# Kernel optimization log

Hardware: AMD Instinct MI355X
Metric: run time of the kernel (lower is better)

## Reference

```python
import jax, jax.numpy as jnp
import numpy as np

MAX_DIST = 20
N_HEADS = 8
LN_EPS = 1e-5


def _layer_norm(x, g, b):
    mu = jnp.mean(x, axis=-1, keepdims=True)
    var = jnp.var(x, axis=-1, keepdims=True)
    return (x - mu) / jnp.sqrt(var + LN_EPS) * g + b


def setup_inputs() -> dict:
    key = jax.random.key(0)
    ks = jax.random.split(key, 12)
    B, N, D, H, F = 8, 1024, 768, N_HEADS, 1024
    w = lambda k, *sh: (jax.random.normal(k, sh, jnp.float32) * 0.02)
    return {
        "x": jax.random.normal(ks[0], (B, N, D), jnp.float32),
        "node_mask": jnp.ones((B, N), jnp.int32),
        "centers": jnp.arange(B * N, dtype=jnp.float32).reshape(B, N),
        "types": jax.random.randint(ks[1], (B, N), 0, 2, jnp.int32),
        # params (torch Linear weights stored transposed as [in, out])
        "qkv_w": w(ks[2], D, 3 * D), "qkv_b": jnp.zeros((3 * D,), jnp.float32),
        "out_w": w(ks[3], D, D), "out_b": jnp.zeros((D,), jnp.float32),
        "ff1_w": w(ks[4], D, F), "ff1_b": jnp.zeros((F,), jnp.float32),
        "ff2_w": w(ks[5], F, D), "ff2_b": jnp.zeros((D,), jnp.float32),
        "ln1_g": jnp.ones((D,), jnp.float32), "ln1_b": jnp.zeros((D,), jnp.float32),
        "ln2_g": jnp.ones((D,), jnp.float32), "ln2_b": jnp.zeros((D,), jnp.float32),
        "rel_emb": w(ks[6], 2 * MAX_DIST + 1, H),  # relative-distance bias table
        "tt": w(ks[7], H, 2, 2),                   # type-pair bias table
    }


def reference(x, node_mask, centers, types,
              qkv_w, qkv_b, out_w, out_b,
              ff1_w, ff1_b, ff2_w, ff2_b,
              ln1_g, ln1_b, ln2_g, ln2_b,
              rel_emb, tt):
    B, N, D = x.shape
    H = rel_emb.shape[1]
    Dh = D // H

    qkv = x @ qkv_w + qkv_b                       # [B,N,3D]
    q, k, v = jnp.split(qkv, 3, axis=-1)
    split = lambda t: t.reshape(B, N, H, Dh).transpose(0, 2, 1, 3)  # [B,H,N,Dh]
    q, k, v = split(q), split(k), split(v)

    scores = jnp.einsum("bhid,bhjd->bhij", q, k) / np.sqrt(Dh).astype(np.float32)

    # relative-position bias: bucket clamped distance into [0, 2*max_dist]
    dist = centers[:, :, None] - centers[:, None, :]              # [B,N,N]
    idx = jnp.round(jnp.clip(dist, -MAX_DIST, MAX_DIST) + MAX_DIST).astype(jnp.int32)
    rb = rel_emb[idx].transpose(0, 3, 1, 2)                       # [B,H,N,N]

    # type-pair bias
    ti = jnp.broadcast_to(types[:, :, None], (B, N, N))
    tj = jnp.broadcast_to(types[:, None, :], (B, N, N))
    tb = tt[:, ti, tj].transpose(1, 0, 2, 3)                      # [B,H,N,N]

    scores = scores + rb + tb
    mask = node_mask[:, None, None, :]                            # [B,1,1,N]
    scores = jnp.where(mask == 0, -jnp.inf, scores)
    att = jax.nn.softmax(scores, axis=-1)
    att = jnp.nan_to_num(att, nan=0.0)

    y = jnp.einsum("bhij,bhjd->bhid", att, v)
    y = y.transpose(0, 2, 1, 3).reshape(B, N, D)
    y = y @ out_w + out_b

    x = _layer_norm(x + y, ln1_g, ln1_b)
    ff = jax.nn.gelu(x @ ff1_w + ff1_b, approximate=False) @ ff2_w + ff2_b
    x = _layer_norm(x + ff, ln2_g, ln2_b)
    return x
```

## Files before the change

### kernel.cpp

```cpp
#include <hip/hip_runtime.h>

typedef short short8 __attribute__((ext_vector_type(8)));
typedef unsigned short ushort8v __attribute__((ext_vector_type(8)));
typedef float f32x4 __attribute__((ext_vector_type(4)));

static __device__ __forceinline__ unsigned short f2b(float f) {
    unsigned int u = __builtin_bit_cast(unsigned int, f);
    unsigned int r = (u + 0x7fffu + ((u >> 16) & 1u)) >> 16;
    return (unsigned short)r;
}
static __device__ __forceinline__ float b2f(unsigned short u) {
    return __builtin_bit_cast(float, (unsigned int)u << 16);
}
static __device__ __forceinline__ float exp2v(float x) {
    float r;
    asm("v_exp_f32 %0, %1" : "=v"(r) : "v"(x));
    return r;
}
static __device__ __forceinline__ unsigned cvt_pk_bf16(float lo, float hi) {
    unsigned r;
    asm("v_cvt_pk_bf16_f32 %0, %1, %2" : "=v"(r) : "v"(lo), "v"(hi));
    return r;
}

__device__ __forceinline__ void gload16(void* lds, const void* g) {
    __builtin_amdgcn_global_load_lds(
        (const __attribute__((address_space(1))) void*)g,
        (__attribute__((address_space(3))) void*)lds, 16, 0, 0);
}

#define L2E 1.4426950408889634f

__global__ __launch_bounds__(256) void prep_kernel(
    const float* __restrict__ x, unsigned short* __restrict__ xb,
    const float* __restrict__ qkv_w, unsigned short* __restrict__ qwT,
    const float* __restrict__ out_w, unsigned short* __restrict__ owT,
    const float* __restrict__ ff1_w, unsigned short* __restrict__ f1T,
    const float* __restrict__ ff2_w, unsigned short* __restrict__ f2T) {
    const int bx = blockIdx.x;
    const int tid = threadIdx.x;
    if (bx < 6144) {
        int i = bx * 256 + tid;
        float4 f = ((const float4*)x)[i];
        ushort4 u;
        u.x = f2b(f.x); u.y = f2b(f.y); u.z = f2b(f.z); u.w = f2b(f.w);
        ((ushort4*)xb)[i] = u;
        return;
    }
    __shared__ float t[32][33];
    int rb = bx - 6144;
    const float* W; unsigned short* Wt; int K, N;
    if (rb < 1728)      { W = qkv_w; Wt = qwT; K = 768;  N = 2304; }
    else if (rb < 2304) { rb -= 1728; W = out_w; Wt = owT; K = 768;  N = 768; }
    else if (rb < 3072) { rb -= 2304; W = ff1_w; Wt = f1T; K = 768;  N = 1024; }
    else                { rb -= 3072; W = ff2_w; Wt = f2T; K = 1024; N = 768; }
    const int nbl = N / 32;
    const int nb = (rb % nbl) * 32, kb = (rb / nbl) * 32;
    const int tx = tid & 31, ty = tid >> 5;
#pragma unroll
    for (int i = 0; i < 32; i += 8)
        t[ty + i][tx] = W[(size_t)(kb + ty + i) * N + nb + tx];
    __syncthreads();
#pragma unroll
    for (int i = 0; i < 32; i += 8)
        Wt[(size_t)(nb + ty + i) * K + kb + tx] = f2b(t[tx][ty + i]);
}

template <int EPI>
__global__ __launch_bounds__(512, 4) void gemm2p(
    const unsigned short* __restrict__ A, const unsigned short* __restrict__ Bt,
    const float* __restrict__ bias, float* __restrict__ outf,
    unsigned short* __restrict__ outb, unsigned short* __restrict__ q_o,
    unsigned short* __restrict__ k_o, unsigned short* __restrict__ v_o,
    int N, int K, int ntn, int NT) {
    __shared__ unsigned short a_lds[2][8192];
    __shared__ unsigned short b_lds[2][8192];
    const int tid = threadIdx.x;
    const int wave = tid >> 6, lane = tid & 63;
    const int lr = lane & 15, lg = lane >> 4;
    const int wm = wave >> 2, wn = wave & 3;
    const int nwg = gridDim.x;
    const int orig = blockIdx.x;
    const int swz = (orig & 7) * (nwg >> 3) + (orig >> 3);
    const int tm = swz / ntn, tn = swz % ntn;

    const unsigned short* srcA[2];
    const unsigned short* srcB[2];
#pragma unroll
    for (int i = 0; i < 2; ++i) {
        int g = i * 512 + tid;
        int row = g >> 3, sl = g & 7;
        int colg = sl ^ (row & 7);
        srcA[i] = A + (size_t)(tm * 128 + row) * K + colg * 8;
        srcB[i] = Bt + (size_t)(tn * 128 + row) * K + colg * 8;
    }
    auto stage = [&](int buf, int k0) {
#pragma unroll
        for (int i = 0; i < 2; ++i) {
            gload16(&a_lds[buf][i * 4096 + wave * 512], srcA[i] + k0);
            gload16(&b_lds[buf][i * 4096 + wave * 512], srcB[i] + k0);
        }
    };

    f32x4 acc[4][2] = {};

    stage(0, 0);
    asm volatile("s_waitcnt vmcnt(0)" ::: "memory");
    __builtin_amdgcn_s_barrier();

    for (int t = 0; t < NT; ++t) {
        const int buf = t & 1;
        if (t + 1 < NT) stage(buf ^ 1, (t + 1) * 64);
#pragma unroll
        for (int ks = 0; ks < 2; ++ks) {
            short8 af[4], bfr[2];
#pragma unroll
            for (int mf = 0; mf < 4; ++mf) {
                int row = wm * 64 + mf * 16 + lr;
                int slot = (ks * 4 + lg) ^ (row & 7);
                af[mf] = *(const short8*)&a_lds[buf][row * 64 + slot * 8];
            }
#pragma unroll
            for (int nf = 0; nf < 2; ++nf) {
                int row = wn * 32 + nf * 16 + lr;
                int slot = (ks * 4 + lg) ^ (row & 7);
                bfr[nf] = *(const short8*)&b_lds[buf][row * 64 + slot * 8];
            }
#pragma unroll
            for (int mf = 0; mf < 4; ++mf)
#pragma unroll
                for (int nf = 0; nf < 2; ++nf)
                    acc[mf][nf] = __builtin_amdgcn_mfma_f32_16x16x32_bf16(af[mf], bfr[nf], acc[mf][nf], 0, 0, 0);
        }
        asm volatile("s_waitcnt vmcnt(0)" ::: "memory");
        __builtin_amdgcn_s_barrier();
    }

#pragma unroll
    for (int nf = 0; nf < 2; ++nf) {
        int gc = tn * 128 + wn * 32 + nf * 16 + lr;
        float bv = bias[gc];
        int part = 0, h = 0, dh = 0;
        if constexpr (EPI == 3) {
            part = gc / 768;
            int cc = gc - part * 768;
            h = cc / 96;
            dh = cc - h * 96;
        }
#pragma unroll
        for (int mf = 0; mf < 4; ++mf) {
            int grb = tm * 128 + wm * 64 + mf * 16 + lg * 4;
            if constexpr (EPI == 3) {
                int b = grb >> 10, n2 = grb & 1023;
                size_t bh = (size_t)(b * 8 + h);
                if (part == 2) {
                    ushort4 wv;
                    wv.x = f2b(acc[mf][nf][0] + bv);
                    wv.y = f2b(acc[mf][nf][1] + bv);
                    wv.z = f2b(acc[mf][nf][2] + bv);
                    wv.w = f2b(acc[mf][nf][3] + bv);
                    *(ushort4*)&v_o[(bh * 96 + dh) * 1024 + n2] = wv;
                } else {
                    unsigned short* dst = (part == 0) ? q_o : k_o;
                    float sc = (part == 0) ? 0.14724445f : 1.f;
#pragma unroll
                    for (int r = 0; r < 4; ++r)
                        dst[(bh * 1024 + n2 + r) * 96 + dh] = f2b((acc[mf][nf][r] + bv) * sc);
                }
            } else {
#pragma unroll
                for (int r = 0; r < 4; ++r) {
                    int gr = grb + r;
                    float v = acc[mf][nf][r] + bv;
                    if constexpr (EPI == 0) {
                        outf[(size_t)gr * N + gc] = v;
                    } else if constexpr (EPI == 1) {
                        outb[(size_t)gr * N + gc] = f2b(v);
                    } else {
                        float gl = 0.5f * v * (1.f + erff(v * 0.70710678f));
                        outb[(size_t)gr * N + gc] = f2b(gl);
                    }
                }
            }
        }
    }
}

__global__ __launch_bounds__(512, 4) void attn_kernel(
    const unsigned short* __restrict__ Qb, const unsigned short* __restrict__ Kb,
    const unsigned short* __restrict__ Vt, const float* __restrict__ centers,
    const int* __restrict__ types, const int* __restrict__ nmask,
    const float* __restrict__ tt, const float* __restrict__ rel_emb,
    unsigned short* __restrict__ Y) {
    __shared__ unsigned short kv_lds[2 * 12288];
    __shared__ unsigned short p_lds[8 * 1024];
    __shared__ float c_lds[1024];
    __shared__ unsigned int bab_lds[1024];
    __shared__ float rel_lds[41];
    __shared__ float cjmm_lds[32];

    const int tid = threadIdx.x;
    const int wave = tid >> 6, lane = tid & 63;
    const int lr = lane & 15, lg = lane >> 4;
    const int bh = blockIdx.x, qb = blockIdx.y;
    const int b = bh >> 3, h = bh & 7;
    const int q0 = qb * 128 + wave * 16;
    const size_t kvbase = (size_t)bh * 1024 * 96;

    c_lds[tid] = centers[b * 1024 + tid];
    c_lds[tid + 512] = centers[b * 1024 + 512 + tid];
    if (tid < 41) rel_lds[tid] = rel_emb[tid * 8 + h] * L2E;
    {
        const float t00 = tt[h * 4], t01 = tt[h * 4 + 1];
        const float t10 = tt[h * 4 + 2], t11 = tt[h * 4 + 3];
#pragma unroll
        for (int i = 0; i < 2; ++i) {
            int j = tid + i * 512;
            int tj = types[b * 1024 + j];
            int mk = nmask[b * 1024 + j];
            float bA = L2E * (t00 + (t01 - t00) * tj) + (mk ? 0.f : -1e30f);
            float bB = L2E * ((t10 - t00) + (t11 - t01 - t10 + t00) * tj);
            bab_lds[j] = (unsigned)f2b(bA) | ((unsigned)f2b(bB) << 16);
        }
    }

    const unsigned short* sbase[3];
    int sstep[3];
#pragma unroll
    for (int it = 0; it < 3; ++it) {
        int g = it * 512 + tid;
        if (g < 768) {
            int ks = g >> 8, rem = g & 255, pr = rem >> 3, sl = rem & 7;
            int so = sl ^ (pr & 7);
            int r = ((so >> 2) << 5) + pr, oct = so & 3;
            sbase[it] = Kb + kvbase + (size_t)r * 96 + ks * 32 + oct * 8;
            sstep[it] = 64 * 96;
        } else {
            int gv = g - 768, pr = gv >> 3, sl = gv & 7;
            int so = sl ^ (pr & 7);
            sbase[it] = Vt + (size_t)(bh * 96 + pr) * 1024 + so * 8;
            sstep[it] = 64;
        }
    }
    auto stage = [&](int bufb, int kt) {
        unsigned short* dst = kv_lds + bufb * 12288;
#pragma unroll
        for (int it = 0; it < 3; ++it)
            gload16(dst + it * 4096 + wave * 512, sbase[it] + (size_t)kt * sstep[it]);
    };

    short8 qa[3];
#pragma unroll
    for (int ks = 0; ks < 3; ++ks)
        qa[ks] = *(const short8*)&Qb[kvbase + (size_t)(q0 + lr) * 96 + ks * 32 + lg * 8];
    short8 qa3 = {};
    {
        int ti0 = types[b * 1024 + q0 + lr];
        if (lg == 0) {
            qa3[0] = (short)0x3F80;
            qa3[1] = ti0 ? (short)0x3F80 : (short)0;
        }
    }
    const float ci20 = centers[b * 1024 + q0 + lr] + 20.f;
    float cimax20 = ci20, cimin20 = ci20;
#pragma unroll
    for (int off = 1; off < 16; off <<= 1) {
        cimax20 = fmaxf(cimax20, __shfl_xor(cimax20, off));
        cimin20 = fminf(cimin20, __shfl_xor(cimin20, off));
    }

    float m_s = -3e30f, l_s = 0.f;
    f32x4 oacc[6] = {};
    unsigned* p32 = (unsigned*)&p_lds[wave * 1024];

    stage(0, 0);
    asm volatile("s_waitcnt lgkmcnt(0)" ::: "memory");
    __builtin_amdgcn_s_barrier();

    if (tid < 256) {
        int ktt = tid >> 4;
        float4 cv = *(const float4*)&c_lds[ktt * 64 + (tid & 15) * 4];
        float mn = fminf(fminf(cv.x, cv.y), fminf(cv.z, cv.w));
        float mx = fmaxf(fmaxf(cv.x, cv.y), fmaxf(cv.z, cv.w));
#pragma unroll
        for (int off = 1; off < 16; off <<= 1) {
            mn = fminf(mn, __shfl_xor(mn, off));
            mx = fmaxf(mx, __shfl_xor(mx, off));
        }
        if ((tid & 15) == 0) { cjmm_lds[ktt] = mn; cjmm_lds[16 + ktt] = mx; }
    }
    asm volatile("s_waitcnt lgkmcnt(0)" ::: "memory");
    const float rel0v = rel_lds[0], rel40v = rel_lds[40];

    for (int kt = 0; kt < 16; ++kt) {
        const int buf = kt & 1;
        if (kt < 15) {
            stage(buf ^ 1, kt + 1);
            asm volatile("s_waitcnt vmcnt(3)" ::: "memory");
        } else {
            asm volatile("s_waitcnt vmcnt(0)" ::: "memory");
        }
        __builtin_amdgcn_s_barrier();
        const unsigned short* kv = kv_lds + buf * 12288;

        f32x4 s[4] = {};
#pragma unroll
        for (int jf = 0; jf < 4; ++jf) {
            int pr = ((jf & 1) << 4) + lr;
            int slp = (((jf >> 1) << 2) + lg) ^ (lr & 7);
#pragma unroll
            for (int ks = 0; ks < 3; ++ks) {
                short8 kf = *(const short8*)&kv[ks * 2048 + pr * 64 + slp * 8];
                s[jf] = __builtin_amdgcn_mfma_f32_16x16x32_bf16(kf, qa[ks], s[jf], 0, 0, 0);
            }
            unsigned vb = bab_lds[kt * 64 + jf * 16 + lr];
            short8 kf3 = {};
            if (lg == 0) {
                kf3[0] = (short)(vb & 0xffffu);
                kf3[1] = (short)(vb >> 16);
            }
            s[jf] = __builtin_amdgcn_mfma_f32_16x16x32_bf16(kf3, qa3, s[jf], 0, 0, 0);
        }

        float re_eff;
        {
            float cjmn = cjmm_lds[kt], cjmx = cjmm_lds[16 + kt];
            bool flatHi = (cimin20 - cjmx >= 40.f);
            bool flatLo = (cimax20 - cjmn <= 0.f);
            if (flatHi || flatLo) {
                re_eff = flatHi ? rel40v : rel0v;
            } else {
                re_eff = 0.f;
#pragma unroll
                for (int jf = 0; jf < 4; ++jf) {
                    float4 cj4 = *(const float4*)&c_lds[kt * 64 + jf * 16 + lg * 4];
                    float cjl[4] = {cj4.x, cj4.y, cj4.z, cj4.w};
#pragma unroll
                    for (int r = 0; r < 4; ++r) {
                        float idxf = __builtin_amdgcn_fmed3f(ci20 - cjl[r], 0.f, 40.f);
                        s[jf][r] += rel_lds[(int)rintf(idxf)];
                    }
                }
            }
        }

        {
            float mlr = s[0][0];
#pragma unroll
            for (int jf = 0; jf < 4; ++jf)
#pragma unroll
                for (int r = 0; r < 4; ++r) mlr = fmaxf(mlr, s[jf][r]);
            float mb = m_s - re_eff;
            if (!__all(mlr <= mb + 8.f)) {
                float mx = fmaxf(mlr, __shfl_xor(mlr, 16));
                mx = fmaxf(mx, __shfl_xor(mx, 32));
                mx += re_eff;
                float mn = fmaxf(m_s, mx);
                float al = exp2v(m_s - mn);
                m_s = mn;
                l_s *= al;
#pragma unroll
                for (int r = 0; r < 4; ++r) {
                    float alr = __shfl(al, lg * 4 + r);
#pragma unroll
                    for (int nf = 0; nf < 6; ++nf) oacc[nf][r] *= alr;
                }
                mb = m_s - re_eff;
            }
            float ls = 0.f;
#pragma unroll
            for (int jf = 0; jf < 4; ++jf)
#pragma unroll
                for (int r = 0; r < 4; ++r) {
                    s[jf][r] = exp2v(s[jf][r] - mb);
                    ls += s[jf][r];
                }
            ls += __shfl_xor(ls, 16);
            ls += __shfl_xor(ls, 32);
            l_s += ls;
        }

#pragma unroll
        for (int jf = 0; jf < 4; ++jf) {
            uint2 w2;
            w2.x = cvt_pk_bf16(s[jf][0], s[jf][1]);
            w2.y = cvt_pk_bf16(s[jf][2], s[jf][3]);
            int gsw = ((jf * 4 + lg) ^ (lr & 14)) * 2;
            *(uint2*)&p32[lr * 32 + gsw] = w2;
        }
        asm volatile("s_waitcnt lgkmcnt(0)" ::: "memory");
        short8 pa[2];
#pragma unroll
        for (int js = 0; js < 2; ++js) {
            int gsw = (((js * 8 + lg * 2) ^ (lr & 14))) * 2;
            pa[js] = *(const short8*)&p32[lr * 32 + gsw];
        }

#pragma unroll
        for (int nf = 0; nf < 6; ++nf) {
            int vrow = nf * 16 + lr;
#pragma unroll
            for (int js = 0; js < 2; ++js) {
                int slp = ((js << 2) + lg) ^ (lr & 7);
                short8 vf = *(const short8*)&kv[6144 + vrow * 64 + slp * 8];
                oacc[nf] = __builtin_amdgcn_mfma_f32_16x16x32_bf16(pa[js], vf, oacc[nf], 0, 0, 0);
            }
        }
        __builtin_amdgcn_s_barrier();
    }

#pragma unroll
    for (int r = 0; r < 4; ++r) {
        float lrow = __shfl(l_s, lg * 4 + r);
        float inv = (lrow > 0.f) ? 1.f / lrow : 0.f;
        int qi = q0 + lg * 4 + r;
#pragma unroll
        for (int nf = 0; nf < 6; ++nf)
            Y[((size_t)b * 1024 + qi) * 768 + h * 96 + nf * 16 + lr] = f2b(oacc[nf][r] * inv);
    }
}

template <bool IN1BF, bool IN2BF>
__global__ __launch_bounds__(384) void ln_kernel(const void* __restrict__ in1,
                                                 const void* __restrict__ in2,
                                                 const float* __restrict__ g,
                                                 const float* __restrict__ be,
                                                 float* __restrict__ of,
                                                 unsigned short* __restrict__ ob) {
    const int tid = threadIdx.x;
    const int half = tid / 192;
    const int t = tid - half * 192;
    const int row = blockIdx.x * 2 + half;
    const size_t base = (size_t)row * 768 + t * 4;
    float a[4], bb[4];
    if (IN1BF) {
        ushort4 u = *(const ushort4*)((const unsigned short*)in1 + base);
        a[0] = b2f(u.x); a[1] = b2f(u.y); a[2] = b2f(u.z); a[3] = b2f(u.w);
    } else {
        float4 u = *(const float4*)((const float*)in1 + base);
        a[0] = u.x; a[1] = u.y; a[2] = u.z; a[3] = u.w;
    }
    if (IN2BF) {
        ushort4 u = *(const ushort4*)((const unsigned short*)in2 + base);
        bb[0] = b2f(u.x); bb[1] = b2f(u.y); bb[2] = b2f(u.z); bb[3] = b2f(u.w);
    } else {
        float4 u = *(const float4*)((const float*)in2 + base);
        bb[0] = u.x; bb[1] = u.y; bb[2] = u.z; bb[3] = u.w;
    }
    float v[4];
#pragma unroll
    for (int i = 0; i < 4; ++i) v[i] = a[i] + bb[i];
    float s1 = v[0] + v[1] + v[2] + v[3];
    float s2 = v[0] * v[0] + v[1] * v[1] + v[2] * v[2] + v[3] * v[3];
#pragma unroll
    for (int off = 32; off > 0; off >>= 1) {
        s1 += __shfl_xor(s1, off);
        s2 += __shfl_xor(s2, off);
    }
    __shared__ float red[12];
    const int wv = tid >> 6;
    if ((tid & 63) == 0) { red[wv] = s1; red[6 + wv] = s2; }
    __syncthreads();
    const int w0 = half * 3;
    s1 = red[w0] + red[w0 + 1] + red[w0 + 2];
    s2 = red[6 + w0] + red[6 + w0 + 1] + red[6 + w0 + 2];
    float mu = s1 * (1.f / 768.f);
    float var = s2 * (1.f / 768.f) - mu * mu;
    float inv = rsqrtf(var + 1e-5f);
    float o[4];
#pragma unroll
    for (int i = 0; i < 4; ++i)
        o[i] = (v[i] - mu) * inv * g[t * 4 + i] + be[t * 4 + i];
    if (of) {
        float4 w = {o[0], o[1], o[2], o[3]};
        *(float4*)(of + base) = w;
    }
    if (ob) {
        ushort4 w = {f2b(o[0]), f2b(o[1]), f2b(o[2]), f2b(o[3])};
        *(ushort4*)(ob + base) = w;
    }
}

extern "C" void kernel_launch(void* const* d_in, const int* in_sizes, int n_in,
                              void* d_out, int out_size, void* d_ws, size_t ws_size,
                              hipStream_t stream) {
    const float* x     = (const float*)d_in[0];
    const int*   nmask = (const int*)d_in[1];
    const float* cent  = (const float*)d_in[2];
    const int*   types = (const int*)d_in[3];
    const float* qkv_w = (const float*)d_in[4];
    const float* qkv_b = (const float*)d_in[5];
    const float* out_w = (const float*)d_in[6];
    const float* out_b = (const float*)d_in[7];
    const float* ff1_w = (const float*)d_in[8];
    const float* ff1_b = (const float*)d_in[9];
    const float* ff2_w = (const float*)d_in[10];
    const float* ff2_b = (const float*)d_in[11];
    const float* ln1_g = (const float*)d_in[12];
    const float* ln1_b = (const float*)d_in[13];
    const float* ln2_g = (const float*)d_in[14];
    const float* ln2_b = (const float*)d_in[15];
    const float* rel   = (const float*)d_in[16];
    const float* ttp   = (const float*)d_in[17];

    char* w = (char*)d_ws;
    auto alloc = [&](size_t bytes) {
        char* p = w;
        w += (bytes + 255) & ~(size_t)255;
        return p;
    };
    unsigned short* xb  = (unsigned short*)alloc(8192ull * 768 * 2);
    unsigned short* yb  = (unsigned short*)alloc(8192ull * 768 * 2);
    unsigned short* qwT = (unsigned short*)alloc(2304ull * 768 * 2);
    unsigned short* owT = (unsigned short*)alloc(768ull * 768 * 2);
    unsigned short* f1T = (unsigned short*)alloc(1024ull * 768 * 2);
    unsigned short* f2T = (unsigned short*)alloc(768ull * 1024 * 2);
    unsigned short* Qb  = (unsigned short*)alloc(64ull * 1024 * 96 * 2);
    unsigned short* Kb  = (unsigned short*)alloc(64ull * 1024 * 96 * 2);
    unsigned short* Vt  = (unsigned short*)alloc(64ull * 96 * 1024 * 2);
    unsigned short* aob = (unsigned short*)alloc(8192ull * 768 * 2);
    unsigned short* h1b = (unsigned short*)alloc(8192ull * 768 * 2);
    unsigned short* ffa = Qb;

    prep_kernel<<<9984, 256, 0, stream>>>(x, xb, qkv_w, qwT, out_w, owT,
                                          ff1_w, f1T, ff2_w, f2T);

    gemm2p<3><<<1152, 512, 0, stream>>>(xb, qwT, qkv_b, nullptr, nullptr,
                                        Qb, Kb, Vt, 2304, 768, 18, 12);
    attn_kernel<<<dim3(64, 8), 512, 0, stream>>>(Qb, Kb, Vt, cent, types, nmask, ttp, rel, yb);
    gemm2p<1><<<384, 512, 0, stream>>>(yb, owT, out_b, nullptr, aob,
                                       nullptr, nullptr, nullptr, 768, 768, 6, 12);
    ln_kernel<true, true><<<4096, 384, 0, stream>>>(xb, aob, ln1_g, ln1_b, nullptr, h1b);
    gemm2p<2><<<512, 512, 0, stream>>>(h1b, f1T, ff1_b, nullptr, ffa,
                                       nullptr, nullptr, nullptr, 1024, 768, 8, 12);
    gemm2p<1><<<384, 512, 0, stream>>>(ffa, f2T, ff2_b, nullptr, aob,
                                       nullptr, nullptr, nullptr, 768, 1024, 6, 16);
    ln_kernel<true, true><<<4096, 384, 0, stream>>>(h1b, aob, ln2_g, ln2_b, (float*)d_out, nullptr);
}
```

Baseline: 180.5 us.

## Switch GEMM to four-stage LDS ring with BK=32 and partial vmcnt waits

The GEMM's double-buffered K=64 tiles become a 4-buffer ring of K=32 tiles, with loads issued three stages ahead. Waits use counted vmcnt instead of draining all loads, and there is one barrier per iteration. The LDS swizzle is adapted to the 32-wide rows. The aim is to hide global-load latency better. The cost is twice as many iterations and barriers, with fewer MFMAs per barrier.

```diff
diff --git a/kernel.cpp b/kernel.cpp
--- a/kernel.cpp
+++ b/kernel.cpp
@@ -67,14 +67,14 @@
 }
 
 template <int EPI>
-__global__ __launch_bounds__(512, 4) void gemm2p(
+__global__ __launch_bounds__(512, 4) void gemm4r(
     const unsigned short* __restrict__ A, const unsigned short* __restrict__ Bt,
     const float* __restrict__ bias, float* __restrict__ outf,
     unsigned short* __restrict__ outb, unsigned short* __restrict__ q_o,
     unsigned short* __restrict__ k_o, unsigned short* __restrict__ v_o,
     int N, int K, int ntn, int NT) {
-    __shared__ unsigned short a_lds[2][8192];
-    __shared__ unsigned short b_lds[2][8192];
+    __shared__ unsigned short a_lds[4][4096];
+    __shared__ unsigned short b_lds[4][4096];
     const int tid = threadIdx.x;
     const int wave = tid >> 6, lane = tid & 63;
     const int lr = lane & 15, lg = lane >> 4;
@@ -84,56 +84,46 @@
     const int swz = (orig & 7) * (nwg >> 3) + (orig >> 3);
     const int tm = swz / ntn, tn = swz % ntn;
 
-    const unsigned short* srcA[2];
-    const unsigned short* srcB[2];
-#pragma unroll
-    for (int i = 0; i < 2; ++i) {
-        int g = i * 512 + tid;
-        int row = g >> 3, sl = g & 7;
-        int colg = sl ^ (row & 7);
-        srcA[i] = A + (size_t)(tm * 128 + row) * K + colg * 8;
-        srcB[i] = Bt + (size_t)(tn * 128 + row) * K + colg * 8;
-    }
-    auto stage = [&](int buf, int k0) {
-#pragma unroll
-        for (int i = 0; i < 2; ++i) {
-            gload16(&a_lds[buf][i * 4096 + wave * 512], srcA[i] + k0);
-            gload16(&b_lds[buf][i * 4096 + wave * 512], srcB[i] + k0);
-        }
+    const int grow = tid >> 2;
+    const int gcol = (tid & 3) ^ ((grow >> 1) & 3);
+    const unsigned short* srcA = A + (size_t)(tm * 128 + grow) * K + gcol * 8;
+    const unsigned short* srcB = Bt + (size_t)(tn * 128 + grow) * K + gcol * 8;
+    auto stage = [&](int buf, int t) {
+        gload16(&a_lds[buf][wave * 512], srcA + t * 32);
+        gload16(&b_lds[buf][wave * 512], srcB + t * 32);
     };
 
     f32x4 acc[4][2] = {};
 
     stage(0, 0);
-    asm volatile("s_waitcnt vmcnt(0)" ::: "memory");
-    __builtin_amdgcn_s_barrier();
+    if (NT > 1) stage(1, 1);
+    if (NT > 2) stage(2, 2);
 
     for (int t = 0; t < NT; ++t) {
-        const int buf = t & 1;
-        if (t + 1 < NT) stage(buf ^ 1, (t + 1) * 64);
-#pragma unroll
-        for (int ks = 0; ks < 2; ++ks) {
-            short8 af[4], bfr[2];
-#pragma unroll
-            for (int mf = 0; mf < 4; ++mf) {
-                int row = wm * 64 + mf * 16 + lr;
-                int slot = (ks * 4 + lg) ^ (row & 7);
-                af[mf] = *(const short8*)&a_lds[buf][row * 64 + slot * 8];
-            }
-#pragma unroll
-            for (int nf = 0; nf < 2; ++nf) {
-                int row = wn * 32 + nf * 16 + lr;
-                int slot = (ks * 4 + lg) ^ (row & 7);
-                bfr[nf] = *(const short8*)&b_lds[buf][row * 64 + slot * 8];
-            }
-#pragma unroll
-            for (int mf = 0; mf < 4; ++mf)
-#pragma unroll
-                for (int nf = 0; nf < 2; ++nf)
-                    acc[mf][nf] = __builtin_amdgcn_mfma_f32_16x16x32_bf16(af[mf], bfr[nf], acc[mf][nf], 0, 0, 0);
-        }
-        asm volatile("s_waitcnt vmcnt(0)" ::: "memory");
+        if (t + 2 < NT)      asm volatile("s_waitcnt vmcnt(4)" ::: "memory");
+        else if (t + 1 < NT) asm volatile("s_waitcnt vmcnt(2)" ::: "memory");
+        else                 asm volatile("s_waitcnt vmcnt(0)" ::: "memory");
         __builtin_amdgcn_s_barrier();
+        if (t + 3 < NT) stage((t + 3) & 3, t + 3);
+        const int buf = t & 3;
+        short8 af[4], bfr[2];
+#pragma unroll
+        for (int mf = 0; mf < 4; ++mf) {
+            int row = wm * 64 + mf * 16 + lr;
+            int slot = lg ^ ((row >> 1) & 3);
+            af[mf] = *(const short8*)&a_lds[buf][row * 32 + slot * 8];
+        }
+#pragma unroll
+        for (int nf = 0; nf < 2; ++nf) {
+            int row = wn * 32 + nf * 16 + lr;
+            int slot = lg ^ ((row >> 1) & 3);
+            bfr[nf] = *(const short8*)&b_lds[buf][row * 32 + slot * 8];
+        }
+#pragma unroll
+        for (int mf = 0; mf < 4; ++mf)
+#pragma unroll
+            for (int nf = 0; nf < 2; ++nf)
+                acc[mf][nf] = __builtin_amdgcn_mfma_f32_16x16x32_bf16(af[mf], bfr[nf], acc[mf][nf], 0, 0, 0);
     }
 
 #pragma unroll
@@ -525,15 +515,15 @@
     prep_kernel<<<9984, 256, 0, stream>>>(x, xb, qkv_w, qwT, out_w, owT,
                                           ff1_w, f1T, ff2_w, f2T);
 
-    gemm2p<3><<<1152, 512, 0, stream>>>(xb, qwT, qkv_b, nullptr, nullptr,
-                                        Qb, Kb, Vt, 2304, 768, 18, 12);
+    gemm4r<3><<<1152, 512, 0, stream>>>(xb, qwT, qkv_b, nullptr, nullptr,
+                                        Qb, Kb, Vt, 2304, 768, 18, 24);
     attn_kernel<<<dim3(64, 8), 512, 0, stream>>>(Qb, Kb, Vt, cent, types, nmask, ttp, rel, yb);
-    gemm2p<1><<<384, 512, 0, stream>>>(yb, owT, out_b, nullptr, aob,
-                                       nullptr, nullptr, nullptr, 768, 768, 6, 12);
+    gemm4r<1><<<384, 512, 0, stream>>>(yb, owT, out_b, nullptr, aob,
+                                       nullptr, nullptr, nullptr, 768, 768, 6, 24);
     ln_kernel<true, true><<<4096, 384, 0, stream>>>(xb, aob, ln1_g, ln1_b, nullptr, h1b);
-    gemm2p<2><<<512, 512, 0, stream>>>(h1b, f1T, ff1_b, nullptr, ffa,
-                                       nullptr, nullptr, nullptr, 1024, 768, 8, 12);
-    gemm2p<1><<<384, 512, 0, stream>>>(ffa, f2T, ff2_b, nullptr, aob,
-                                       nullptr, nullptr, nullptr, 768, 1024, 6, 16);
+    gemm4r<2><<<512, 512, 0, stream>>>(h1b, f1T, ff1_b, nullptr, ffa,
+                                       nullptr, nullptr, nullptr, 1024, 768, 8, 24);
+    gemm4r<1><<<384, 512, 0, stream>>>(ffa, f2T, ff2_b, nullptr, aob,
+                                       nullptr, nullptr, nullptr, 768, 1024, 6, 32);
     ln_kernel<true, true><<<4096, 384, 0, stream>>>(h1b, aob, ln2_g, ln2_b, (float*)d_out, nullptr);
 }
```

Result: slower. 195.8 us (+8.5%).
